# Kernel optimization log

Measured on AMD Instinct MI355X. Metric: run time of the kernel, lower is better.

The kernel has to match this reference:

```python
import jax, jax.numpy as jnp
import numpy as np

EPS = 1e-8
B, S1, S2, D, H, L, NCLS = 4, 256, 256, 300, 256, 10, 22
AGG_IN = 2 + 3 * 2 * L  # cos max/mean + (maxpool, attentive, max-attentive) x (fw,bw) x l = 62


def _lstm_dir(x, Wih, Whh, b):
    # x: (batch, seq, in); PyTorch gate order i, f, g, o
    pre = jnp.einsum('bsd,gd->bsg', x, Wih) + b
    h0 = jnp.zeros((x.shape[0], Whh.shape[1]), x.dtype)
    def step(carry, p):
        h, c = carry
        g = p + h @ Whh.T
        i, f, gg, o = jnp.split(g, 4, axis=-1)
        c = jax.nn.sigmoid(f) * c + jax.nn.sigmoid(i) * jnp.tanh(gg)
        h = jax.nn.sigmoid(o) * jnp.tanh(c)
        return (h, c), h
    (hT, _), hs = jax.lax.scan(step, (h0, h0), jnp.swapaxes(pre, 0, 1))
    return jnp.swapaxes(hs, 0, 1), hT


def bilstm(x, Wf, Uf, bf, Wb, Ub, bb):
    hs_f, hT_f = _lstm_dir(x, Wf, Uf, bf)
    hs_b, hT_b = _lstm_dir(x[:, ::-1], Wb, Ub, bb)
    return jnp.concatenate([hs_f, hs_b[:, ::-1]], -1), hT_f, hT_b


def div_small(n, d):
    return n / jnp.where(d > EPS, d, EPS)


def cos_matrix(v1, v2):
    # (b,p,h),(b,q,h) -> (b,p,q) cosine similarity matrix (attention())
    a = jnp.einsum('bph,bqh->bpq', v1, v2)
    d = jnp.linalg.norm(v1, axis=-1)[:, :, None] * jnp.linalg.norm(v2, axis=-1)[:, None, :]
    return div_small(a, d)


def mp_match(v1, v2, w):
    # mp_matching_func: cosine over h of (w*v1, w*v2) per perspective -> (b,s,l)
    w2 = w * w
    num = jnp.einsum('lh,bsh,bsh->bsl', w2, v1, v2)
    n1 = jnp.sqrt(jnp.einsum('lh,bsh->bsl', w2, v1 * v1))
    n2 = jnp.sqrt(jnp.einsum('lh,bsh->bsl', w2, v2 * v2))
    return num / jnp.maximum(n1 * n2, EPS)


def mp_match_pairwise(v1, v2, w):
    # mp_matching_func_pairwise -> (b,p,q,l)
    v1w = v1[:, None] * w[None, :, None]  # (b,l,p,h)
    v2w = v2[:, None] * w[None, :, None]  # (b,l,q,h)
    n = jnp.einsum('blph,blqh->blpq', v1w, v2w)
    d = jnp.linalg.norm(v1w, axis=-1)[:, :, :, None] * jnp.linalg.norm(v2w, axis=-1)[:, :, None, :]
    return jnp.transpose(div_small(n, d), (0, 2, 3, 1))


def bimpm_forward(left, right,
                  ctx_Wih_f, ctx_Whh_f, ctx_b_f, ctx_Wih_b, ctx_Whh_b, ctx_b_b,
                  agg_Wih_f, agg_Whh_f, agg_b_f, agg_Wih_b, agg_Whh_b, agg_b_b,
                  mp_w3, mp_w4, mp_w5, mp_w6, mp_w7, mp_w8,
                  fc1_W, fc1_b, fc2_W, fc2_b):
    cp, _, _ = bilstm(left, ctx_Wih_f, ctx_Whh_f, ctx_b_f, ctx_Wih_b, ctx_Whh_b, ctx_b_b)
    ch, _, _ = bilstm(right, ctx_Wih_f, ctx_Whh_f, ctx_b_f, ctx_Wih_b, ctx_Whh_b, ctx_b_b)
    p_fw, p_bw = jnp.split(cp, 2, -1)  # (b,p,H) each
    h_fw, h_bw = jnp.split(ch, 2, -1)  # (b,q,H) each
    att_fw = cos_matrix(p_fw, h_fw)  # also the cosine_sim used for max/mean match
    att_bw = cos_matrix(p_bw, h_bw)
    mv1 = [att_fw.max(2, keepdims=True), att_fw.mean(2, keepdims=True)]
    mv2 = [att_fw.max(1)[..., None], att_fw.mean(1)[..., None]]
    # maxpool match
    mm_fw = mp_match_pairwise(p_fw, h_fw, mp_w3)
    mm_bw = mp_match_pairwise(p_bw, h_bw, mp_w4)
    mv1 += [mm_fw.max(2), mm_bw.max(2)]
    mv2 += [mm_fw.max(1), mm_bw.max(1)]
    # attentive + max-attentive match
    def att_stats(att, vp, vh):
        mean_h = div_small(jnp.einsum('bpq,bqh->bph', att, vh), att.sum(2, keepdims=True))
        mean_p = div_small(jnp.einsum('bpq,bph->bqh', att, vp), att.sum(1)[..., None])
        max_h = jnp.max(att[..., None] * vh[:, None, :, :], axis=2)  # (b,p,H)
        max_p = jnp.max(att[..., None] * vp[:, :, None, :], axis=1)  # (b,q,H)
        return mean_h, mean_p, max_h, max_p
    mh_fw, mpv_fw, xh_fw, xp_fw = att_stats(att_fw, p_fw, h_fw)
    mh_bw, mpv_bw, xh_bw, xp_bw = att_stats(att_bw, p_bw, h_bw)
    mv1 += [mp_match(p_fw, mh_fw, mp_w5), mp_match(p_bw, mh_bw, mp_w6),
            mp_match(p_fw, xh_fw, mp_w7), mp_match(p_bw, xh_bw, mp_w8)]
    mv2 += [mp_match(h_fw, mpv_fw, mp_w5), mp_match(h_bw, mpv_bw, mp_w6),
            mp_match(h_fw, xp_fw, mp_w7), mp_match(h_bw, xp_bw, mp_w8)]
    mv_p = jnp.concatenate(mv1, -1)  # (b,p,62)
    mv_h = jnp.concatenate(mv2, -1)  # (b,q,62)
    _, ap_f, ap_b = bilstm(mv_p, agg_Wih_f, agg_Whh_f, agg_b_f, agg_Wih_b, agg_Whh_b, agg_b_b)
    _, ah_f, ah_b = bilstm(mv_h, agg_Wih_f, agg_Whh_f, agg_b_f, agg_Wih_b, agg_Whh_b, agg_b_b)
    l1, l2 = left.shape[1], right.shape[1]
    lengths = jnp.broadcast_to(jnp.array([l1 / (l1 + l2), l2 / (l1 + l2)], left.dtype), (left.shape[0], 2))
    x = jnp.concatenate([ap_f, ap_b, ah_f, ah_b, lengths, left.mean(1), right.mean(1)], -1)
    x = jnp.tanh(x @ fc1_W.T + fc1_b)
    return x @ fc2_W.T + fc2_b


def setup_inputs():
    ks = jax.random.split(jax.random.key(0), 20)
    f = lambda i, shape, s=0.1: jax.random.normal(ks[i], shape, jnp.float32) * s
    return {
        'left': jax.random.normal(ks[0], (B, S1, D), jnp.float32),
        'right': jax.random.normal(ks[1], (B, S2, D), jnp.float32),
        'ctx_Wih_f': f(2, (4 * H, D)), 'ctx_Whh_f': f(3, (4 * H, H)), 'ctx_b_f': jnp.zeros((4 * H,), jnp.float32),
        'ctx_Wih_b': f(4, (4 * H, D)), 'ctx_Whh_b': f(5, (4 * H, H)), 'ctx_b_b': jnp.zeros((4 * H,), jnp.float32),
        'agg_Wih_f': f(6, (4 * H, AGG_IN)), 'agg_Whh_f': f(7, (4 * H, H)), 'agg_b_f': jnp.zeros((4 * H,), jnp.float32),
        'agg_Wih_b': f(8, (4 * H, AGG_IN)), 'agg_Whh_b': f(9, (4 * H, H)), 'agg_b_b': jnp.zeros((4 * H,), jnp.float32),
        'mp_w3': f(10, (L, H), 0.3), 'mp_w4': f(11, (L, H), 0.3), 'mp_w5': f(12, (L, H), 0.3),
        'mp_w6': f(13, (L, H), 0.3), 'mp_w7': f(14, (L, H), 0.3), 'mp_w8': f(15, (L, H), 0.3),
        'fc1_W': f(16, (2 * H, 4 * H + 2 + 2 * D), 0.01), 'fc1_b': jnp.zeros((2 * H,), jnp.float32),
        'fc2_W': f(17, (NCLS, 2 * H), 0.01), 'fc2_b': jnp.zeros((NCLS,), jnp.float32),
    }


def reference(left, right, ctx_Wih_f, ctx_Whh_f, ctx_b_f, ctx_Wih_b, ctx_Whh_b, ctx_b_b,
              agg_Wih_f, agg_Whh_f, agg_b_f, agg_Wih_b, agg_Whh_b, agg_b_b,
              mp_w3, mp_w4, mp_w5, mp_w6, mp_w7, mp_w8, fc1_W, fc1_b, fc2_W, fc2_b):
    return bimpm_forward(left, right, ctx_Wih_f, ctx_Whh_f, ctx_b_f, ctx_Wih_b, ctx_Whh_b, ctx_b_b,
                         agg_Wih_f, agg_Whh_f, agg_b_f, agg_Wih_b, agg_Whh_b, agg_b_b,
                         mp_w3, mp_w4, mp_w5, mp_w6, mp_w7, mp_w8, fc1_W, fc1_b, fc2_W, fc2_b)
```

## Files before the change

### kernel.cpp

```cpp
#include <hip/hip_runtime.h>
#include <hip/hip_bf16.h>
#include <math.h>

#define EPSV 1e-8f

__device__ __forceinline__ float dsmall(float d){ return d > EPSV ? d : EPSV; }
__device__ __forceinline__ float sigf(float x){ return 1.f/(1.f+expf(-x)); }

__global__ __launch_bounds__(1024) void k_transpose2(const float* __restrict__ WF,
                                                     const float* __restrict__ WB,
                                                     float* __restrict__ WT0,
                                                     float* __restrict__ WT1){
  const float* W = blockIdx.z ? WB : WF;
  float* WT = blockIdx.z ? WT1 : WT0;
  __shared__ float t[32][33];
  int rb = blockIdx.y*32, cb = blockIdx.x*32;
  int r = rb + threadIdx.y, c = cb + threadIdx.x;
  t[threadIdx.y][threadIdx.x] = W[(size_t)r*256 + c];
  __syncthreads();
  int rr = cb + threadIdx.y, cc = rb + threadIdx.x;
  WT[(size_t)rr*1024 + cc] = t[threadIdx.x][threadIdx.y];
}

__global__ __launch_bounds__(256) void k_proj(
    const float* __restrict__ left, const float* __restrict__ right,
    const float* __restrict__ WihF, const float* __restrict__ WihB,
    const float* __restrict__ bF, const float* __restrict__ bB,
    float* __restrict__ PREf, float* __restrict__ PREb)
{
  const int z = blockIdx.z, zo = z >> 1, zi = z & 1;
  const float* A = zo ? right : left;
  const float* B = zi ? WihB : WihF;
  const float* bias = zi ? bB : bF;
  float* C = (zi ? PREb : PREf) + (size_t)zo*1048576;
  const int K = 300;

  __shared__ float As[16][68];
  __shared__ float Bs[16][68];
  const int mb = blockIdx.y*64, nb = blockIdx.x*64;
  const int tid = threadIdx.x;
  const int tx = tid & 15, ty = tid >> 4;

  float acc[4][4];
  #pragma unroll
  for (int i=0;i<4;i++)
    #pragma unroll
    for (int j=0;j<4;j++) acc[i][j] = 0.f;

  for (int kt = 0; kt < K; kt += 16) {
    int ka = tid & 15, ma = tid >> 4;
    #pragma unroll
    for (int q=0;q<4;q++){
      int m = ma + q*16;
      float v = 0.f, bvv = 0.f;
      if (kt+ka < K){
        v = A[(size_t)(mb+m)*300 + kt+ka];
        bvv = B[(size_t)(nb+m)*300 + kt+ka];
      }
      As[ka][m] = v; Bs[ka][m] = bvv;
    }
    __syncthreads();
    #pragma unroll
    for (int k=0;k<16;k++){
      float a[4], bv[4];
      #pragma unroll
      for (int i=0;i<4;i++) a[i] = As[k][ty*4+i];
      #pragma unroll
      for (int j=0;j<4;j++) bv[j] = Bs[k][tx*4+j];
      #pragma unroll
      for (int i=0;i<4;i++)
        #pragma unroll
        for (int j=0;j<4;j++) acc[i][j] += a[i]*bv[j];
    }
    __syncthreads();
  }
  #pragma unroll
  for (int i=0;i<4;i++){
    int m = mb + ty*4 + i;
    #pragma unroll
    for (int j=0;j<4;j++){
      int n = nb + tx*4 + j;
      C[(size_t)m*1024 + n] = acc[i][j] + bias[n];
    }
  }
}

__global__ __launch_bounds__(256) void k_aggproj(
    const float* __restrict__ MV_,
    const float* __restrict__ WihF, const float* __restrict__ WihB,
    const float* __restrict__ bF, const float* __restrict__ bB,
    float* __restrict__ PREf, float* __restrict__ PREb)
{
  const int zi = blockIdx.z;
  const float* B = zi ? WihB : WihF;
  const float* bias = zi ? bB : bF;
  float* C = zi ? PREb : PREf;
  const int K = 62;

  __shared__ float As[16][68];
  __shared__ float Bs[16][68];
  const int mb = blockIdx.y*64, nb = blockIdx.x*64;
  const int tid = threadIdx.x;
  const int tx = tid & 15, ty = tid >> 4;

  float acc[4][4];
  #pragma unroll
  for (int i=0;i<4;i++)
    #pragma unroll
    for (int j=0;j<4;j++) acc[i][j] = 0.f;

  for (int kt = 0; kt < K; kt += 16) {
    int ka = tid & 15, ma = tid >> 4;
    #pragma unroll
    for (int q=0;q<4;q++){
      int m = ma + q*16;
      float v = 0.f, bvv = 0.f;
      if (kt+ka < K){
        v = MV_[(size_t)(mb+m)*62 + kt+ka];
        bvv = B[(size_t)(nb+m)*62 + kt+ka];
      }
      As[ka][m] = v; Bs[ka][m] = bvv;
    }
    __syncthreads();
    #pragma unroll
    for (int k=0;k<16;k++){
      float a[4], bv[4];
      #pragma unroll
      for (int i=0;i<4;i++) a[i] = As[k][ty*4+i];
      #pragma unroll
      for (int j=0;j<4;j++) bv[j] = Bs[k][tx*4+j];
      #pragma unroll
      for (int i=0;i<4;i++)
        #pragma unroll
        for (int j=0;j<4;j++) acc[i][j] += a[i]*bv[j];
    }
    __syncthreads();
  }
  #pragma unroll
  for (int i=0;i<4;i++){
    int m = mb + ty*4 + i;
    #pragma unroll
    for (int j=0;j<4;j++){
      int n = nb + tx*4 + j;
      C[(size_t)m*1024 + n] = acc[i][j] + bias[n];
    }
  }
}

__global__ __launch_bounds__(256) void k_att(
    const float* __restrict__ HS_, const float* __restrict__ NORM_,
    float* __restrict__ ATT_)
{
  const int z = blockIdx.z;
  const int d = z >> 2, b = z & 3;
  const float* A = HS_ + d*256 + (size_t)b*131072;
  const float* B = HS_ + 524288 + d*256 + (size_t)b*131072;
  const float* Uv = NORM_ + (size_t)b*512 + d*256;
  const float* Vv = NORM_ + (size_t)(4+b)*512 + d*256;
  float* C = ATT_ + (size_t)z*65536;

  __shared__ float As[16][68];
  __shared__ float Bs[16][68];
  const int mb = blockIdx.y*64, nb = blockIdx.x*64;
  const int tid = threadIdx.x;
  const int tx = tid & 15, ty = tid >> 4;

  float acc[4][4];
  #pragma unroll
  for (int i=0;i<4;i++)
    #pragma unroll
    for (int j=0;j<4;j++) acc[i][j] = 0.f;

  for (int kt = 0; kt < 256; kt += 16) {
    int ka = tid & 15, ma = tid >> 4;
    #pragma unroll
    for (int q=0;q<4;q++){
      int m = ma + q*16;
      As[ka][m] = A[(size_t)(mb+m)*512 + kt+ka];
      Bs[ka][m] = B[(size_t)(nb+m)*512 + kt+ka];
    }
    __syncthreads();
    #pragma unroll
    for (int k=0;k<16;k++){
      float a[4], bv[4];
      #pragma unroll
      for (int i=0;i<4;i++) a[i] = As[k][ty*4+i];
      #pragma unroll
      for (int j=0;j<4;j++) bv[j] = Bs[k][tx*4+j];
      #pragma unroll
      for (int i=0;i<4;i++)
        #pragma unroll
        for (int j=0;j<4;j++) acc[i][j] += a[i]*bv[j];
    }
    __syncthreads();
  }
  #pragma unroll
  for (int i=0;i<4;i++){
    int m = mb + ty*4 + i;
    float um = Uv[m];
    #pragma unroll
    for (int j=0;j<4;j++){
      int n = nb + tx*4 + j;
      C[(size_t)m*256 + n] = acc[i][j] / dsmall(um * Vv[n]);
    }
  }
}

__global__ __launch_bounds__(256) void k_attstat(
    const float* __restrict__ ATT_, const float* __restrict__ HS_,
    const float* __restrict__ RS_, const float* __restrict__ CS_,
    float* __restrict__ MEANH_, float* __restrict__ XH_,
    float* __restrict__ MEANP_, float* __restrict__ XP_)
{
  const int z16 = blockIdx.z;
  const int var = z16 >> 3;
  const int z = z16 & 7;
  const int d = z >> 2, b = z & 3;
  const float* A = ATT_ + (size_t)z*65536;
  const float* B = (var ? HS_ : HS_ + 524288) + d*256 + (size_t)b*131072;
  const float* U = (var ? CS_ : RS_) + z*256;
  float* C1 = (var ? MEANP_ : MEANH_) + (size_t)z*65536;
  float* C2 = (var ? XP_    : XH_   ) + (size_t)z*65536;

  __shared__ float As[16][68];
  __shared__ float Bs[16][68];
  const int mb = blockIdx.y*64, nb = blockIdx.x*64;
  const int tid = threadIdx.x;
  const int tx = tid & 15, ty = tid >> 4;

  float asum[4][4], amax[4][4];
  #pragma unroll
  for (int i=0;i<4;i++)
    #pragma unroll
    for (int j=0;j<4;j++){ asum[i][j]=0.f; amax[i][j]=-INFINITY; }

  for (int kt = 0; kt < 256; kt += 16) {
    if (var == 0) {
      int ka = tid & 15, ma = tid >> 4;
      #pragma unroll
      for (int q=0;q<4;q++)
        As[ka][ma+q*16] = A[(size_t)(mb+ma+q*16)*256 + kt+ka];
    } else {
      int ma = tid & 63, ka = tid >> 6;
      #pragma unroll
      for (int q=0;q<4;q++)
        As[ka+q*4][ma] = A[(size_t)(kt+ka+q*4)*256 + mb+ma];
    }
    {
      int nbi = tid & 63, kb = tid >> 6;
      #pragma unroll
      for (int q=0;q<4;q++)
        Bs[kb+q*4][nbi] = B[(size_t)(kt+kb+q*4)*512 + nb+nbi];
    }
    __syncthreads();
    #pragma unroll
    for (int k=0;k<16;k++){
      float a[4], bv[4];
      #pragma unroll
      for (int i=0;i<4;i++) a[i] = As[k][ty*4+i];
      #pragma unroll
      for (int j=0;j<4;j++) bv[j] = Bs[k][tx*4+j];
      #pragma unroll
      for (int i=0;i<4;i++)
        #pragma unroll
        for (int j=0;j<4;j++){
          float p = a[i]*bv[j];
          asum[i][j] += p;
          amax[i][j] = fmaxf(amax[i][j], p);
        }
    }
    __syncthreads();
  }
  #pragma unroll
  for (int i=0;i<4;i++){
    int m = mb + ty*4 + i;
    float ud = dsmall(U[m]);
    #pragma unroll
    for (int j=0;j<4;j++){
      int n = nb + tx*4 + j;
      C1[(size_t)m*256 + n] = asum[i][j] / ud;
      C2[(size_t)m*256 + n] = amax[i][j];
    }
  }
}

__global__ __launch_bounds__(256) void k_pmm2(
    const float* __restrict__ HS_,
    const float* __restrict__ w3, const float* __restrict__ w4,
    const float* __restrict__ WN1_, const float* __restrict__ WN2_,
    float* __restrict__ PARTR, float* __restrict__ PARTC)
{
  const int z = blockIdx.z;
  const int dir = z >= 40;
  const int zz = z - dir*40;
  const int bq = zz / 10, l = zz % 10;
  const float* A = HS_ + dir*256 + (size_t)bq*131072;
  const float* B = HS_ + 524288 + dir*256 + (size_t)bq*131072;
  const float* Wv = (dir ? w4 : w3) + l*256;
  const float* U = WN1_ + dir*10240 + bq*2560 + l*256;
  const float* V = WN2_ + dir*10240 + bq*2560 + l*256;

  __shared__ float As[16][68];
  __shared__ float Bs[16][68];
  const int mb = blockIdx.y*64, nb = blockIdx.x*64;
  const int tid = threadIdx.x;
  const int tx = tid & 15, ty = tid >> 4;

  float acc[4][4];
  #pragma unroll
  for (int i=0;i<4;i++)
    #pragma unroll
    for (int j=0;j<4;j++) acc[i][j] = 0.f;

  for (int kt = 0; kt < 256; kt += 16) {
    int ka = tid & 15, ma = tid >> 4;
    float w = Wv[kt+ka]; float w2 = w*w;
    #pragma unroll
    for (int q=0;q<4;q++){
      As[ka][ma+q*16] = A[(size_t)(mb+ma+q*16)*512 + kt+ka] * w2;
      Bs[ka][ma+q*16] = B[(size_t)(nb+ma+q*16)*512 + kt+ka];
    }
    __syncthreads();
    #pragma unroll
    for (int k=0;k<16;k++){
      float a[4], bv[4];
      #pragma unroll
      for (int i=0;i<4;i++) a[i] = As[k][ty*4+i];
      #pragma unroll
      for (int j=0;j<4;j++) bv[j] = Bs[k][tx*4+j];
      #pragma unroll
      for (int i=0;i<4;i++)
        #pragma unroll
        for (int j=0;j<4;j++) acc[i][j] += a[i]*bv[j];
    }
    __syncthreads();
  }
  float um[4], vn[4];
  #pragma unroll
  for (int i=0;i<4;i++) um[i] = U[mb + ty*4 + i];
  #pragma unroll
  for (int j=0;j<4;j++) vn[j] = V[nb + tx*4 + j];
  float c[4][4];
  #pragma unroll
  for (int i=0;i<4;i++)
    #pragma unroll
    for (int j=0;j<4;j++) c[i][j] = acc[i][j] / dsmall(um[i]*vn[j]);

  float rm[4];
  #pragma unroll
  for (int i=0;i<4;i++){
    rm[i] = fmaxf(fmaxf(c[i][0], c[i][1]), fmaxf(c[i][2], c[i][3]));
    rm[i] = fmaxf(rm[i], __shfl_xor(rm[i], 1, 64));
    rm[i] = fmaxf(rm[i], __shfl_xor(rm[i], 2, 64));
    rm[i] = fmaxf(rm[i], __shfl_xor(rm[i], 4, 64));
    rm[i] = fmaxf(rm[i], __shfl_xor(rm[i], 8, 64));
  }
  if ((tid & 15) == 0){
    #pragma unroll
    for (int i=0;i<4;i++)
      PARTR[((size_t)z*4 + blockIdx.x)*256 + mb + ty*4 + i] = rm[i];
  }
  __syncthreads();
  float* colp = &As[0][0];
  #pragma unroll
  for (int j=0;j<4;j++)
    colp[ty*64 + tx*4 + j] = fmaxf(fmaxf(c[0][j], c[1][j]), fmaxf(c[2][j], c[3][j]));
  __syncthreads();
  if (tid < 64){
    float m = colp[tid];
    #pragma unroll
    for (int r=1;r<16;r++) m = fmaxf(m, colp[r*64 + tid]);
    PARTC[((size_t)z*4 + blockIdx.y)*256 + nb + tid] = m;
  }
}

__global__ void k_pcomb(const float* __restrict__ PARTR, const float* __restrict__ PARTC,
                        float* __restrict__ MMRo, float* __restrict__ MMCo){
  int z = blockIdx.x, i = threadIdx.x;
  size_t b0 = (size_t)z*4*256 + i;
  float r = fmaxf(fmaxf(PARTR[b0], PARTR[b0+256]), fmaxf(PARTR[b0+512], PARTR[b0+768]));
  float c = fmaxf(fmaxf(PARTC[b0], PARTC[b0+256]), fmaxf(PARTC[b0+512], PARTC[b0+768]));
  MMRo[(size_t)z*256 + i] = r;
  MMCo[(size_t)z*256 + i] = c;
}

__global__ __launch_bounds__(256, 1) void k_scanaux(
    const float* __restrict__ PREf, const float* __restrict__ PREb,
    const float* __restrict__ WTf, const float* __restrict__ WTb,
    float* __restrict__ Hbuf, int* __restrict__ flg,
    float* __restrict__ HSo, float* __restrict__ HTo,
    int do_aux,
    const float* __restrict__ fc1W, float* __restrict__ W1T,
    const float* __restrict__ aWhhF, float* __restrict__ WTaggF,
    const float* __restrict__ aWhhB, float* __restrict__ WTaggB,
    const float* __restrict__ left, const float* __restrict__ right,
    float* __restrict__ XM)
{
  __shared__ float Wl[256][128];
  __shared__ float hl[256][2];
  __shared__ float red[4][8][40];

  const int bx = blockIdx.x;
  const int tid = threadIdx.x;

  if (bx >= 64) {
    if (!do_aux) return;
    float (*tl)[33] = (float(*)[33])Wl;
    const int aux = bx - 64;
    for (int u = aux; u < 816 + 512 + 8; u += 64) {
      if (u < 816) {
        int tI = u % 16, tJ = u / 16;
        int r0 = tI*32, c0 = tJ*32;
        for (int e = tid; e < 1024; e += 256) {
          int rr = e >> 5, cc = e & 31;
          int c = c0 + cc;
          tl[rr][cc] = (c < 1626) ? fc1W[(size_t)(r0+rr)*1626 + c] : 0.f;
        }
        __syncthreads();
        for (int e = tid; e < 1024; e += 256) {
          int cc = e >> 5, rr = e & 31;
          int c = c0 + cc;
          if (c < 1626) W1T[(size_t)c*512 + r0 + rr] = tl[rr][cc];
        }
        __syncthreads();
      } else if (u < 1328) {
        int u2 = u - 816;
        const float* S = (u2 >= 256) ? aWhhB : aWhhF;
        float* D = (u2 >= 256) ? WTaggB : WTaggF;
        int tile = u2 & 255;
        int r0 = (tile >> 3)*32, c0 = (tile & 7)*32;
        for (int e = tid; e < 1024; e += 256) {
          int rr = e >> 5, cc = e & 31;
          tl[rr][cc] = S[(size_t)(r0+rr)*256 + c0 + cc];
        }
        __syncthreads();
        for (int e = tid; e < 1024; e += 256) {
          int cc = e >> 5, rr = e & 31;
          D[(size_t)(c0+cc)*1024 + r0 + rr] = tl[rr][cc];
        }
        __syncthreads();
      } else {
        int m = u - 1328;
        int b = m & 3, sideR = m >> 2;
        const float* src = sideR ? right : left;
        for (int ch = tid; ch < 300; ch += 256) {
          float s = 0.f;
          for (int t = 0; t < 256; t++) s += src[((size_t)(b*256+t))*300 + ch];
          XM[b*600 + sideR*300 + ch] = s * (1.f/256.f);
        }
      }
    }
    return;
  }

  const int team = bx & 7;
  const int d   = team >> 2;
  const int sq0 = (team & 3)*2;
  const int wg  = bx >> 3;
  const float* PRE = d ? PREb : PREf;
  const float* WT  = d ? WTb  : WTf;
  float* Hb = Hbuf + (size_t)team*1024;
  int* fl = flg + team*256;

  const int kc = tid >> 5;
  const int gq = tid & 31;
  const int as = tid >> 5;
  const int aj = tid & 31;

  for (int e = tid; e < 256*128; e += 256) {
    int k = e >> 7, c = e & 127;
    Wl[k][c] = WT[(size_t)k*1024 + (c>>5)*256 + wg*32 + (c&31)];
  }
  for (int e = tid; e < 512; e += 256) ((float*)hl)[e] = 0.f;
  float cst = 0.f;
  __syncthreads();

  for (int tt = 0; tt < 256; ++tt) {
    const int t = d ? 255 - tt : tt;
    const int wp = tt & 1;
    const int sp = (tt + 1) & 1;

    float pre0=0.f, pre1=0.f, pre2=0.f, pre3=0.f;
    if (tid < 64) {
      const size_t pbase = ((size_t)((sq0+as)*256 + t))*1024 + wg*32 + aj;
      pre0 = PRE[pbase];       pre1 = PRE[pbase + 256];
      pre2 = PRE[pbase + 512]; pre3 = PRE[pbase + 768];
    }

    if (tt > 0 && kc != wg) {
      const int* flp = &fl[kc*32];
      while (__hip_atomic_load(flp, __ATOMIC_RELAXED, __HIP_MEMORY_SCOPE_AGENT) < tt)
        __builtin_amdgcn_s_sleep(1);
      const unsigned long long* srcu =
          (const unsigned long long*)&Hb[sp*512 + (kc*32 + gq)*2];
      unsigned long long u0 = __hip_atomic_load(srcu, __ATOMIC_RELAXED, __HIP_MEMORY_SCOPE_AGENT);
      *(unsigned long long*)&hl[kc*32 + gq][0] = u0;
    }

    float acc[2][4];
    #pragma unroll
    for (int s=0;s<2;s++){ acc[s][0]=0.f; acc[s][1]=0.f; acc[s][2]=0.f; acc[s][3]=0.f; }
    #pragma unroll 8
    for (int kk = 0; kk < 32; ++kk) {
      const int k = kc*32 + kk;
      float4 w  = *(const float4*)&Wl[k][gq*4];
      float2 ha = *(const float2*)&hl[k][0];
      acc[0][0] += ha.x*w.x; acc[0][1] += ha.x*w.y; acc[0][2] += ha.x*w.z; acc[0][3] += ha.x*w.w;
      acc[1][0] += ha.y*w.x; acc[1][1] += ha.y*w.y; acc[1][2] += ha.y*w.z; acc[1][3] += ha.y*w.w;
    }
    #pragma unroll
    for (int s=0;s<2;s++)
      #pragma unroll
      for (int c2=0;c2<4;c2++)
        acc[s][c2] += __shfl_xor(acc[s][c2], 32, 64);
    if ((tid & 32) == 0) {
      const int kp = kc >> 1;
      #pragma unroll
      for (int s=0;s<2;s++)
        #pragma unroll
        for (int c2=0;c2<4;c2++)
          red[kp][s*4+c2][gq] = acc[s][c2];
    }
    __syncthreads();

    float hreg = 0.f;
    if (tid < 64) {
      float g[4];
      #pragma unroll
      for (int gt=0; gt<4; ++gt) {
        const int c = gt*32 + aj;
        const int gqq = c >> 2, cc = c & 3;
        const int ii = as*4 + cc;
        g[gt] = red[0][ii][gqq] + red[1][ii][gqq] + red[2][ii][gqq] + red[3][ii][gqq];
      }
      g[0] += pre0; g[1] += pre1; g[2] += pre2; g[3] += pre3;
      const float ig = sigf(g[0]), fg = sigf(g[1]), gg = tanhf(g[2]), og = sigf(g[3]);
      cst = fg*cst + ig*gg;
      hreg = og*tanhf(cst);
      hl[wg*32 + aj][as] = hreg;
      __hip_atomic_store(&Hb[wp*512 + (wg*32 + aj)*2 + as], hreg,
                         __ATOMIC_RELAXED, __HIP_MEMORY_SCOPE_AGENT);
    }
    __syncthreads();

    if (tid == 0)
      __hip_atomic_store(&fl[wg*32], tt+1, __ATOMIC_RELAXED, __HIP_MEMORY_SCOPE_AGENT);

    if (tid < 64) {
      if (HSo) HSo[((size_t)((sq0+as)*256 + t))*512 + d*256 + wg*32 + aj] = hreg;
      if (HTo && tt == 255) HTo[((size_t)((sq0+as)*2 + d))*256 + wg*32 + aj] = hreg;
    }
  }
}

__global__ __launch_bounds__(256) void k_norms(const float* __restrict__ HS_,
                                               const float* __restrict__ w3, const float* __restrict__ w4,
                                               float* __restrict__ NORM_,
                                               float* __restrict__ WN1_, float* __restrict__ WN2_){
  const int bx = blockIdx.x;
  int lane = threadIdx.x & 63;
  if (bx < 1024) {
    int r = bx*4 + (threadIdx.x >> 6);
    int seq = r >> 9, d = (r >> 8) & 1, i = r & 255;
    const float* row = HS_ + ((size_t)(seq*256 + i))*512 + d*256;
    float s = 0.f;
    #pragma unroll
    for (int q=0;q<4;q++){ float v = row[lane + 64*q]; s += v*v; }
    for (int off=32; off; off>>=1) s += __shfl_xor(s, off, 64);
    if (lane == 0) NORM_[r] = sqrtf(s);
  } else {
    int rid = (bx-1024)*4 + (threadIdx.x >> 6);
    int side = rid / 20480; int rem = rid % 20480;
    int d = rem / 10240; int rem2 = rem % 10240;
    int b = rem2 / 2560; int l = (rem2 / 256) % 10; int i = rem2 & 255;
    int seq = side ? 4+b : b;
    const float* row = HS_ + ((size_t)(seq*256 + i))*512 + d*256;
    const float* w = (d ? w4 : w3) + l*256;
    float s = 0.f;
    #pragma unroll
    for (int q=0;q<4;q++){ float wv = w[lane+64*q]; float v = row[lane+64*q]; s += wv*wv*v*v; }
    for (int off=32; off; off>>=1) s += __shfl_xor(s, off, 64);
    if (lane == 0) (side ? WN2_ : WN1_)[rem] = sqrtf(s);
  }
}

__global__ __launch_bounds__(256) void k_redcomb(const float* __restrict__ ATT_,
                                                 float* __restrict__ RS_, float* __restrict__ RMAX_,
                                                 float* __restrict__ CS_, float* __restrict__ CMAX_){
  const int bx = blockIdx.x;
  if (bx < 512) {
    int r = bx*4 + (threadIdx.x >> 6);
    int lane = threadIdx.x & 63;
    const float* row = ATT_ + (size_t)r*256;
    float s = 0.f, m = -INFINITY;
    #pragma unroll
    for (int q=0;q<4;q++){ float v = row[lane + 64*q]; s += v; m = fmaxf(m,v); }
    for (int off=32; off; off>>=1){ s += __shfl_xor(s,off,64); m = fmaxf(m, __shfl_xor(m,off,64)); }
    if (lane == 0){ RS_[r] = s; RMAX_[r] = m; }
  } else {
    int z = bx - 512;
    const float* in = ATT_ + (size_t)z*65536;
    int j = threadIdx.x;
    float s = 0.f, m = -INFINITY;
    for (int r=0;r<256;r++){ float v = in[(size_t)r*256 + j]; s += v; m = fmaxf(m,v); }
    CS_[z*256 + j] = s;
    CMAX_[z*256 + j] = m;
  }
}

__global__ __launch_bounds__(256) void k_mv(
    const float* __restrict__ HS_, const float* __restrict__ MEANH_, const float* __restrict__ MEANP_,
    const float* __restrict__ XH_, const float* __restrict__ XP_,
    const float* __restrict__ RS_, const float* __restrict__ RMAX_,
    const float* __restrict__ CS_, const float* __restrict__ CMAX_,
    const float* __restrict__ MMR_, const float* __restrict__ MMC_,
    const float* __restrict__ w5, const float* __restrict__ w6,
    const float* __restrict__ w7, const float* __restrict__ w8,
    float* __restrict__ MV_)
{
  const int blk = blockIdx.x;
  const int side = blk >> 10, b = (blk >> 8) & 3, i = blk & 255;
  const int wv = threadIdx.x >> 6, lane = threadIdx.x & 63;
  float* mvrow = MV_ + (size_t)blk*62;

  if (threadIdx.x == 0){
    const float* rmax = side ? CMAX_ : RMAX_;
    const float* rsum = side ? CS_   : RS_;
    mvrow[0] = rmax[b*256 + i];
    mvrow[1] = rsum[b*256 + i] * (1.f/256.f);
  }
  if (threadIdx.x < 20){
    int dd = threadIdx.x / 10, l = threadIdx.x % 10;
    const float* mm = side ? MMC_ : MMR_;
    mvrow[2 + dd*10 + l] = mm[dd*10240 + (b*10 + l)*256 + i];
  }
  const int d = wv & 1;
  const int seq = side ? 4+b : b;
  const float* arow = HS_ + ((size_t)(seq*256 + i))*512 + d*256;
  const float* Mside = side ? MEANP_ : MEANH_;
  const float* Xside = side ? XP_ : XH_;
  const float* brow = (wv < 2 ? Mside : Xside) + (size_t)d*262144 + (size_t)b*65536 + (size_t)i*256;
  const float* wp = (wv==0) ? w5 : (wv==1) ? w6 : (wv==2) ? w7 : w8;

  float av[4], bv[4];
  #pragma unroll
  for (int q=0;q<4;q++){ av[q] = arow[lane+64*q]; bv[q] = brow[lane+64*q]; }
  for (int l=0;l<10;l++){
    const float* wrow = wp + l*256;
    float s1=0.f, s2=0.f, s3=0.f;
    #pragma unroll
    for (int q=0;q<4;q++){
      float w = wrow[lane+64*q]; float w2v = w*w;
      s1 += w2v*av[q]*bv[q]; s2 += w2v*av[q]*av[q]; s3 += w2v*bv[q]*bv[q];
    }
    for (int off=32; off; off>>=1){
      s1 += __shfl_xor(s1,off,64); s2 += __shfl_xor(s2,off,64); s3 += __shfl_xor(s3,off,64);
    }
    if (lane == 0) mvrow[22 + wv*10 + l] = s1 / fmaxf(sqrtf(s2)*sqrtf(s3), EPSV);
  }
}

__global__ __launch_bounds__(512) void k_fc12(const float* __restrict__ HT_,
                                              const float* __restrict__ XM,
                                              const float* __restrict__ W1T,
                                              const float* __restrict__ b1,
                                              const float* __restrict__ W2,
                                              const float* __restrict__ b2,
                                              float* __restrict__ out){
  __shared__ float x[1626];
  __shared__ float xs2[512];
  int b = blockIdx.x, t = threadIdx.x;
  if (t < 256){
    x[t]       = HT_[(b*2+0)*256 + t];
    x[256+t]   = HT_[(b*2+1)*256 + t];
    x[512+t]   = HT_[((4+b)*2+0)*256 + t];
    x[768+t]   = HT_[((4+b)*2+1)*256 + t];
  }
  if (t == 0){ x[1024] = 0.5f; x[1025] = 0.5f; }
  if (t < 300){ x[1026+t] = XM[b*600 + t]; x[1326+t] = XM[b*600 + 300 + t]; }
  __syncthreads();
  float acc = b1[t];
  for (int k=0;k<1626;k++) acc += x[k]*W1T[(size_t)k*512 + t];
  xs2[t] = tanhf(acc);
  __syncthreads();
  if (t < 22){
    float o = b2[t];
    const float* wr = W2 + (size_t)t*512;
    for (int k=0;k<512;k++) o += xs2[k]*wr[k];
    out[b*22 + t] = o;
  }
}

extern "C" void kernel_launch(void* const* d_in, const int* in_sizes, int n_in,
                              void* d_out, int out_size, void* d_ws, size_t ws_size,
                              hipStream_t stream) {
  const float* left  = (const float*)d_in[0];
  const float* right = (const float*)d_in[1];
  const float* cWihF = (const float*)d_in[2];
  const float* cWhhF = (const float*)d_in[3];
  const float* cbF   = (const float*)d_in[4];
  const float* cWihB = (const float*)d_in[5];
  const float* cWhhB = (const float*)d_in[6];
  const float* cbB   = (const float*)d_in[7];
  const float* aWihF = (const float*)d_in[8];
  const float* aWhhF = (const float*)d_in[9];
  const float* abF   = (const float*)d_in[10];
  const float* aWihB = (const float*)d_in[11];
  const float* aWhhB = (const float*)d_in[12];
  const float* abB   = (const float*)d_in[13];
  const float* w3 = (const float*)d_in[14];
  const float* w4 = (const float*)d_in[15];
  const float* w5 = (const float*)d_in[16];
  const float* w6 = (const float*)d_in[17];
  const float* w7 = (const float*)d_in[18];
  const float* w8 = (const float*)d_in[19];
  const float* fc1W = (const float*)d_in[20];
  const float* fc1b = (const float*)d_in[21];
  const float* fc2W = (const float*)d_in[22];
  const float* fc2b = (const float*)d_in[23];
  float* out = (float*)d_out;
  float* ws = (float*)d_ws;

  float* WT    = ws;
  float* PREf  = ws + 1048576;
  float* PREb  = ws + 3145728;
  float* HS    = ws + 5242880;
  float* NORM  = ws + 6291456;
  float* ATT   = ws + 6295552;
  float* RS    = ws + 6819840;
  float* RMAX  = ws + 6821888;
  float* CS    = ws + 6823936;
  float* CMAX  = ws + 6825984;
  float* MEANH = ws + 6828032;
  float* MEANP = ws + 7352320;
  float* XH    = ws + 7876608;
  float* XP    = ws + 8400896;
  float* WN1   = ws + 8925184;
  float* WN2   = ws + 8945664;
  float* MM    = ws + 8966144;
  float* MMR   = ws + 11587584;
  float* MMC   = ws + 11608064;
  float* MV    = ws + 11628544;
  float* HT    = ws + 11755520;
  float* XM    = ws + 11759616;
  float* W1T   = ws + 11764064;

  float* HXB  = MM;
  int*   FLG  = (int*)(MM + 8192);
  float* PARTR= MM;
  float* PARTC= MM + 81920;

  k_transpose2<<<dim3(8,32,2), dim3(32,32), 0, stream>>>(cWhhF, cWhhB, WT, WT + 262144);

  k_proj<<<dim3(16,16,4),256,0,stream>>>(left, right, cWihF, cWihB, cbF, cbB, PREf, PREb);

  hipMemsetAsync(FLG, 0, 2048*sizeof(int), stream);
  k_scanaux<<<128,256,0,stream>>>(PREf, PREb, WT, WT+262144, HXB, FLG, HS, nullptr,
                                  1, fc1W, W1T, aWhhF, WT+524288, aWhhB, WT+786432,
                                  left, right, XM);

  k_norms<<<11264,256,0,stream>>>(HS, w3, w4, NORM, WN1, WN2);

  k_att<<<dim3(4,4,8),256,0,stream>>>(HS, NORM, ATT);

  k_redcomb<<<520,256,0,stream>>>(ATT, RS, RMAX, CS, CMAX);

  k_attstat<<<dim3(4,4,16),256,0,stream>>>(ATT, HS, RS, CS, MEANH, XH, MEANP, XP);

  k_pmm2<<<dim3(4,4,80),256,0,stream>>>(HS, w3, w4, WN1, WN2, PARTR, PARTC);
  k_pcomb<<<80,256,0,stream>>>(PARTR, PARTC, MMR, MMC);

  k_mv<<<2048,256,0,stream>>>(HS, MEANH, MEANP, XH, XP, RS, RMAX, CS, CMAX,
                              MMR, MMC, w5, w6, w7, w8, MV);

  k_aggproj<<<dim3(16,32,2),256,0,stream>>>(MV, aWihF, aWihB, abF, abB, PREf, PREb);

  hipMemsetAsync(FLG, 0, 2048*sizeof(int), stream);
  k_scanaux<<<128,256,0,stream>>>(PREf, PREb, WT+524288, WT+786432, HXB, FLG, nullptr, HT,
                                  0, fc1W, W1T, aWhhF, WT+524288, aWhhB, WT+786432,
                                  left, right, XM);

  k_fc12<<<4,512,0,stream>>>(HT, XM, W1T, fc1b, fc2W, fc2b, out);
}
```

Measured before the change: 1.631 ms.

## Split LSTM scan teams to one sequence each, doubling scan workgroups

The persistent LSTM scan now gives each team of eight workgroups a single sequence instead of two, so the scan uses 128 workgroups (16 teams) instead of 64. The per-step matvec, reduction buffer and exchanged hidden-state buffers shrink to one sequence, which cuts per-step compute latency on the serial critical path. In exchange, twice as many workgroups must stay co-resident and poll flags, the Wl weight slice is loaded twice as often in total, and the flag and H buffers are resized to match.

```diff
diff --git a/kernel.cpp b/kernel.cpp
--- a/kernel.cpp
+++ b/kernel.cpp
@@ -397,16 +397,16 @@
     float* __restrict__ XM)
 {
   __shared__ float Wl[256][128];
-  __shared__ float hl[256][2];
-  __shared__ float red[4][8][40];
+  __shared__ float hl[256];
+  __shared__ float red[4][4][40];
 
   const int bx = blockIdx.x;
   const int tid = threadIdx.x;
 
-  if (bx >= 64) {
+  if (bx >= 128) {
     if (!do_aux) return;
     float (*tl)[33] = (float(*)[33])Wl;
-    const int aux = bx - 64;
+    const int aux = bx - 128;
     for (int u = aux; u < 816 + 512 + 8; u += 64) {
       if (u < 816) {
         int tI = u % 16, tJ = u / 16;
@@ -453,25 +453,24 @@
     return;
   }
 
-  const int team = bx & 7;
-  const int d   = team >> 2;
-  const int sq0 = (team & 3)*2;
-  const int wg  = bx >> 3;
+  const int team = bx & 15;
+  const int d  = team >> 3;
+  const int sq = team & 7;
+  const int wg = bx >> 4;
   const float* PRE = d ? PREb : PREf;
   const float* WT  = d ? WTb  : WTf;
-  float* Hb = Hbuf + (size_t)team*1024;
+  float* Hb = Hbuf + (size_t)team*512;
   int* fl = flg + team*256;
 
   const int kc = tid >> 5;
   const int gq = tid & 31;
-  const int as = tid >> 5;
   const int aj = tid & 31;
 
   for (int e = tid; e < 256*128; e += 256) {
     int k = e >> 7, c = e & 127;
     Wl[k][c] = WT[(size_t)k*1024 + (c>>5)*256 + wg*32 + (c&31)];
   }
-  for (int e = tid; e < 512; e += 256) ((float*)hl)[e] = 0.f;
+  if (tid < 256) hl[tid] = 0.f;
   float cst = 0.f;
   __syncthreads();
 
@@ -481,8 +480,8 @@
     const int sp = (tt + 1) & 1;
 
     float pre0=0.f, pre1=0.f, pre2=0.f, pre3=0.f;
-    if (tid < 64) {
-      const size_t pbase = ((size_t)((sq0+as)*256 + t))*1024 + wg*32 + aj;
+    if (tid < 32) {
+      const size_t pbase = ((size_t)(sq*256 + t))*1024 + wg*32 + aj;
       pre0 = PRE[pbase];       pre1 = PRE[pbase + 256];
       pre2 = PRE[pbase + 512]; pre3 = PRE[pbase + 768];
     }
@@ -491,54 +490,45 @@
       const int* flp = &fl[kc*32];
       while (__hip_atomic_load(flp, __ATOMIC_RELAXED, __HIP_MEMORY_SCOPE_AGENT) < tt)
         __builtin_amdgcn_s_sleep(1);
-      const unsigned long long* srcu =
-          (const unsigned long long*)&Hb[sp*512 + (kc*32 + gq)*2];
-      unsigned long long u0 = __hip_atomic_load(srcu, __ATOMIC_RELAXED, __HIP_MEMORY_SCOPE_AGENT);
-      *(unsigned long long*)&hl[kc*32 + gq][0] = u0;
-    }
-
-    float acc[2][4];
-    #pragma unroll
-    for (int s=0;s<2;s++){ acc[s][0]=0.f; acc[s][1]=0.f; acc[s][2]=0.f; acc[s][3]=0.f; }
+      float v = __hip_atomic_load(&Hb[sp*256 + kc*32 + gq],
+                                  __ATOMIC_RELAXED, __HIP_MEMORY_SCOPE_AGENT);
+      hl[kc*32 + gq] = v;
+    }
+
+    float acc[4] = {0.f, 0.f, 0.f, 0.f};
     #pragma unroll 8
     for (int kk = 0; kk < 32; ++kk) {
       const int k = kc*32 + kk;
-      float4 w  = *(const float4*)&Wl[k][gq*4];
-      float2 ha = *(const float2*)&hl[k][0];
-      acc[0][0] += ha.x*w.x; acc[0][1] += ha.x*w.y; acc[0][2] += ha.x*w.z; acc[0][3] += ha.x*w.w;
-      acc[1][0] += ha.y*w.x; acc[1][1] += ha.y*w.y; acc[1][2] += ha.y*w.z; acc[1][3] += ha.y*w.w;
-    }
-    #pragma unroll
-    for (int s=0;s<2;s++)
-      #pragma unroll
-      for (int c2=0;c2<4;c2++)
-        acc[s][c2] += __shfl_xor(acc[s][c2], 32, 64);
+      float4 w = *(const float4*)&Wl[k][gq*4];
+      float h = hl[k];
+      acc[0] += h*w.x; acc[1] += h*w.y; acc[2] += h*w.z; acc[3] += h*w.w;
+    }
+    #pragma unroll
+    for (int c2=0;c2<4;c2++)
+      acc[c2] += __shfl_xor(acc[c2], 32, 64);
     if ((tid & 32) == 0) {
       const int kp = kc >> 1;
       #pragma unroll
-      for (int s=0;s<2;s++)
-        #pragma unroll
-        for (int c2=0;c2<4;c2++)
-          red[kp][s*4+c2][gq] = acc[s][c2];
+      for (int c2=0;c2<4;c2++)
+        red[kp][c2][gq] = acc[c2];
     }
     __syncthreads();
 
     float hreg = 0.f;
-    if (tid < 64) {
+    if (tid < 32) {
       float g[4];
       #pragma unroll
       for (int gt=0; gt<4; ++gt) {
         const int c = gt*32 + aj;
         const int gqq = c >> 2, cc = c & 3;
-        const int ii = as*4 + cc;
-        g[gt] = red[0][ii][gqq] + red[1][ii][gqq] + red[2][ii][gqq] + red[3][ii][gqq];
+        g[gt] = red[0][cc][gqq] + red[1][cc][gqq] + red[2][cc][gqq] + red[3][cc][gqq];
       }
       g[0] += pre0; g[1] += pre1; g[2] += pre2; g[3] += pre3;
       const float ig = sigf(g[0]), fg = sigf(g[1]), gg = tanhf(g[2]), og = sigf(g[3]);
       cst = fg*cst + ig*gg;
       hreg = og*tanhf(cst);
-      hl[wg*32 + aj][as] = hreg;
-      __hip_atomic_store(&Hb[wp*512 + (wg*32 + aj)*2 + as], hreg,
+      hl[wg*32 + aj] = hreg;
+      __hip_atomic_store(&Hb[wp*256 + wg*32 + aj], hreg,
                          __ATOMIC_RELAXED, __HIP_MEMORY_SCOPE_AGENT);
     }
     __syncthreads();
@@ -546,9 +536,9 @@
     if (tid == 0)
       __hip_atomic_store(&fl[wg*32], tt+1, __ATOMIC_RELAXED, __HIP_MEMORY_SCOPE_AGENT);
 
-    if (tid < 64) {
-      if (HSo) HSo[((size_t)((sq0+as)*256 + t))*512 + d*256 + wg*32 + aj] = hreg;
-      if (HTo && tt == 255) HTo[((size_t)((sq0+as)*2 + d))*256 + wg*32 + aj] = hreg;
+    if (tid < 32) {
+      if (HSo) HSo[((size_t)(sq*256 + t))*512 + d*256 + wg*32 + aj] = hreg;
+      if (HTo && tt == 255) HTo[((size_t)(sq*2 + d))*256 + wg*32 + aj] = hreg;
     }
   }
 }
@@ -754,8 +744,8 @@
 
   k_proj<<<dim3(16,16,4),256,0,stream>>>(left, right, cWihF, cWihB, cbF, cbB, PREf, PREb);
 
-  hipMemsetAsync(FLG, 0, 2048*sizeof(int), stream);
-  k_scanaux<<<128,256,0,stream>>>(PREf, PREb, WT, WT+262144, HXB, FLG, HS, nullptr,
+  hipMemsetAsync(FLG, 0, 4096*sizeof(int), stream);
+  k_scanaux<<<192,256,0,stream>>>(PREf, PREb, WT, WT+262144, HXB, FLG, HS, nullptr,
                                   1, fc1W, W1T, aWhhF, WT+524288, aWhhB, WT+786432,
                                   left, right, XM);
 
@@ -775,8 +765,8 @@
 
   k_aggproj<<<dim3(16,32,2),256,0,stream>>>(MV, aWihF, aWihB, abF, abB, PREf, PREb);
 
-  hipMemsetAsync(FLG, 0, 2048*sizeof(int), stream);
-  k_scanaux<<<128,256,0,stream>>>(PREf, PREb, WT+524288, WT+786432, HXB, FLG, nullptr, HT,
+  hipMemsetAsync(FLG, 0, 4096*sizeof(int), stream);
+  k_scanaux<<<192,256,0,stream>>>(PREf, PREb, WT+524288, WT+786432, HXB, FLG, nullptr, HT,
                                   0, fc1W, W1T, aWhhF, WT+524288, aWhhB, WT+786432,
                                   left, right, XM);
 
```

After: 1.357 ms. 1.2x faster.
